# Performance work log

Hardware: AMD Instinct MI355X
Metric: run time of the kernel (lower is better)

The kernel has to match this reference:

```python
import jax, jax.numpy as jnp
import numpy as np

B = 32           # graphs in batch
N_PER = 512      # nodes per graph
N = B * N_PER    # 16384 total nodes (block-diagonal batched graph)
E = N * 16       # 262144 edges
D_IN = 128
D_OUT = 128
ASSIGN = 2048    # total clusters = B * K
K = ASSIGN // B  # 64 clusters per graph


def setup_inputs() -> dict:
    key = jax.random.key(0)
    ks = jax.random.split(key, 6)
    h = jax.random.normal(ks[0], (N, D_IN), jnp.float32)
    # edges confined within each graph -> block-diagonal batched adjacency
    gid = jnp.repeat(jnp.arange(B), E // B)
    edge_src = (jax.random.randint(ks[1], (E,), 0, N_PER) + gid * N_PER).astype(jnp.int32)
    edge_dst = (jax.random.randint(ks[2], (E,), 0, N_PER) + gid * N_PER).astype(jnp.int32)
    # GraphSage NodeApply linears: Linear(2*in, out)
    stdv_f = 1.0 / np.sqrt(2 * D_IN)
    W_feat = jax.random.uniform(ks[3], (2 * D_IN, D_OUT), jnp.float32, -stdv_f, stdv_f)
    b_feat = jnp.zeros((D_OUT,), jnp.float32)
    W_pool = jax.random.uniform(ks[4], (2 * D_IN, ASSIGN), jnp.float32, -stdv_f, stdv_f)
    b_pool = jnp.zeros((ASSIGN,), jnp.float32)
    return {"h": h, "W_feat": W_feat, "b_feat": b_feat,
            "W_pool": W_pool, "b_pool": b_pool,
            "edge_src": edge_src, "edge_dst": edge_dst}


def _graphsage(h, W, b, src, dst):
    # mean aggregation over in-neighbors (dropout=0, batch_norm off)
    msg = jax.ops.segment_sum(h[src], dst, num_segments=N)          # [N, d_in]
    deg = jax.ops.segment_sum(jnp.ones((src.shape[0],), h.dtype), dst, num_segments=N)
    h_neigh = msg / jnp.maximum(deg, 1.0)[:, None]
    bundle = jnp.concatenate([h, h_neigh], axis=1) @ W + b          # [N, d_out]
    # F.normalize(p=2, dim=1) then activation, as in GraphSage NodeApply
    norm = jnp.linalg.norm(bundle, axis=1, keepdims=True)
    bundle = bundle / jnp.maximum(norm, 1e-12)
    return jax.nn.relu(bundle)


def _forward(h, W_feat, b_feat, W_pool, b_pool, src, dst):
    feat = _graphsage(h, W_feat, b_feat, src, dst)       # [N, D_OUT]
    assign = _graphsage(h, W_pool, b_pool, src, dst)     # [N, ASSIGN]
    # block-diagonal mask: node i of graph g may only assign to g's K clusters
    gid_n = jnp.arange(N) // N_PER                       # [N]
    gid_c = jnp.arange(ASSIGN) // K                      # [ASSIGN]
    mask = (gid_n[:, None] == gid_c[None, :]).astype(jnp.float32)
    # masked_softmax with memory_efficient=False
    s = jax.nn.softmax(assign * mask, axis=-1) * mask
    s = s / (s.sum(axis=-1, keepdims=True) + 1e-13)      # [N, ASSIGN]
    h_new = s.T @ feat                                   # [ASSIGN, D_OUT]
    # adj_new = S^T A S without densifying A: (A S)[dst] += S[src]
    a_s = jax.ops.segment_sum(s[src], dst, num_segments=N)
    adj_new = s.T @ a_s                                  # [ASSIGN, ASSIGN]
    return adj_new, h_new


def reference(h, W_feat, b_feat, W_pool, b_pool, edge_src, edge_dst):
    return _forward(h, W_feat, b_feat, W_pool, b_pool, edge_src, edge_dst)
```

## Files before the change

kernel.cpp:

```cpp
#include <hip/hip_runtime.h>

#define NB   32
#define NPER 512
#define NN   16384
#define EE   262144
#define DD   128
#define AS   2048
#define KC   64

using short8   = __attribute__((ext_vector_type(8))) short;
using floatx4  = __attribute__((ext_vector_type(4))) float;
using ushort4v = __attribute__((ext_vector_type(4))) unsigned short;

typedef __attribute__((address_space(3))) unsigned int lds_u32;
typedef const __attribute__((address_space(1))) unsigned int gbl_u32;

static __device__ __forceinline__ void gload16(const unsigned short* g, unsigned short* l) {
    __builtin_amdgcn_global_load_lds((gbl_u32*)g, (lds_u32*)l, 16, 0, 0);
}

static __device__ __forceinline__ float bits2f(unsigned int u) {
    union { unsigned int i; float f; } z; z.i = u << 16; return z.f;
}
static __device__ __forceinline__ unsigned short f2b(float x) {
    union { float f; unsigned int u; } v; v.f = x;
    unsigned int r = v.u + 0x7fffu + ((v.u >> 16) & 1u);
    return (unsigned short)(r >> 16);
}

union PrepSMem {
    unsigned short fT[128 * 136];
    float tl[32][33];
};
__global__ void prep_kernel(const float* __restrict__ h, unsigned short* __restrict__ bundle,
                            unsigned short* __restrict__ hT, const int* __restrict__ esrc,
                            const int* __restrict__ edst, unsigned int* __restrict__ Acnt,
                            const float* __restrict__ Wf, const float* __restrict__ Wp,
                            unsigned short* __restrict__ WfT, unsigned short* __restrict__ WpT,
                            unsigned short* __restrict__ Wpb) {
    __shared__ PrepSMem sm;
    int b = blockIdx.x, t = threadIdx.x;
    if (b < 128) {
        int node0 = b * 128;
        int r = t >> 1, hf = t & 1;
        const float4* h4 = reinterpret_cast<const float4*>(h + (size_t)(node0 + r) * 128 + hf * 64);
        unsigned short* bo = bundle + (size_t)(node0 + r) * 256 + hf * 64;
#pragma unroll
        for (int i = 0; i < 16; i++) {
            float4 v = h4[i];
            ushort4v o = { f2b(v.x), f2b(v.y), f2b(v.z), f2b(v.w) };
            *reinterpret_cast<ushort4v*>(bo + 4 * i) = o;
            int c = hf * 64 + 4 * i;
            sm.fT[(c + 0) * 136 + r] = o.x;
            sm.fT[(c + 1) * 136 + r] = o.y;
            sm.fT[(c + 2) * 136 + r] = o.z;
            sm.fT[(c + 3) * 136 + r] = o.w;
        }
        __syncthreads();
        int c = t >> 1, nh = t & 1;
        const uint4* src = reinterpret_cast<const uint4*>(&sm.fT[c * 136 + nh * 64]);
        uint4* dst = reinterpret_cast<uint4*>(hT + (size_t)c * NN + node0 + nh * 64);
#pragma unroll
        for (int i = 0; i < 8; i++) dst[i] = src[i];
    } else if (b < 1152) {
        int e = (b - 128) * 256 + t;
        int d = edst[e], sl = esrc[e] & 511;
        int idx = d * 512 + sl;
        atomicAdd(&Acnt[idx >> 2], 1u << (8 * (idx & 3)));
    } else if (b < 1696) {
        int tb = b - 1152;
        int bx = tb % 68, by = tb / 68;
        int tx = t & 31, ty = t >> 5;
        const float* in; unsigned short* out; int C, cb;
        if (bx < DD / 32) { in = Wf; out = WfT; C = DD; cb = bx; }
        else              { in = Wp; out = WpT; C = AS; cb = bx - DD / 32; }
        int c0 = cb * 32, r0 = by * 32;
        for (int i = 0; i < 4; i++)
            sm.tl[ty + 8 * i][tx] = in[(size_t)(r0 + ty + 8 * i) * C + c0 + tx];
        __syncthreads();
        for (int i = 0; i < 4; i++)
            out[(size_t)(c0 + ty + 8 * i) * 256 + r0 + tx] = f2b(sm.tl[tx][ty + 8 * i]);
    } else {
        int gid = (b - 1696) * 256 + t;
        float4 v = reinterpret_cast<const float4*>(Wp)[gid];
        ushort4v o = { f2b(v.x), f2b(v.y), f2b(v.z), f2b(v.w) };
        *reinterpret_cast<ushort4v*>(&Wpb[(size_t)gid * 4]) = o;
    }
}

__global__ __launch_bounds__(256) void conv_kernel(
    const unsigned int* __restrict__ Acnt, unsigned short* __restrict__ Aadj,
    float* __restrict__ invdeg, const unsigned short* __restrict__ Wpb,
    const float* __restrict__ Wp, const float* __restrict__ bp,
    float* __restrict__ Gf, float* __restrict__ uF, float* __restrict__ cF) {
    __shared__ alignas(16) unsigned short glA[4096];
    __shared__ alignas(16) unsigned short glB[4096];
    __shared__ float gcred[4];
    int t = threadIdx.x, b = blockIdx.x;
    if (b < 2048) {
        int row = b * 8 + (t >> 5);
        int u = t & 31;
        uint4 w = reinterpret_cast<const uint4*>(Acnt)[(size_t)row * 32 + u];
        unsigned int wa[4] = { w.x, w.y, w.z, w.w };
        unsigned short out[16];
        float sum = 0.f;
#pragma unroll
        for (int i = 0; i < 4; i++) {
#pragma unroll
            for (int bb = 0; bb < 4; bb++) {
                float fv = (float)((wa[i] >> (8 * bb)) & 0xffu);
                sum += fv;
                out[4 * i + bb] = f2b(fv);
            }
        }
        unsigned int pw[8];
#pragma unroll
        for (int i = 0; i < 8; i++)
            pw[i] = (unsigned int)out[2 * i] | ((unsigned int)out[2 * i + 1] << 16);
        uint4* dst = reinterpret_cast<uint4*>(Aadj + (size_t)row * 512 + u * 16);
        uint4 s0 = { pw[0], pw[1], pw[2], pw[3] }, s1 = { pw[4], pw[5], pw[6], pw[7] };
        dst[0] = s0; dst[1] = s1;
#pragma unroll
        for (int d = 1; d < 32; d <<= 1) sum += __shfl_xor(sum, d, 64);
        if (u == 0) invdeg[row] = 1.0f / fmaxf(sum, 1.0f);
        return;
    }
    int b2 = b - 2048;
    int ks = b2 >> 2, ti = (b2 >> 1) & 1, tj = b2 & 1;
    int wv = t >> 6, lane = t & 63;
    int mw = wv >> 1, nw = wv & 1, q = lane >> 4, lm = lane & 15;
    int rowS0 = t >> 2,         cS0 = (t & 3) ^ ((rowS0 >> 1) & 3);
    int rowS1 = (t + 256) >> 2, cS1 = ((t + 256) & 3) ^ ((rowS1 >> 1) & 3);
    int swz = q ^ ((lm >> 1) & 3);
    floatx4 acc[4][4];
#pragma unroll
    for (int mi = 0; mi < 4; mi++)
#pragma unroll
        for (int ni = 0; ni < 4; ni++) acc[mi][ni] = (floatx4)0.f;
    for (int ki = 0; ki < 16; ki++) {
        int k0 = ks * 512 + ki * 32;
        gload16(Wpb + (size_t)(ti * 128 + rowS0) * 2048 + k0 + 8 * cS0, &glA[t * 8]);
        gload16(Wpb + (size_t)(ti * 128 + rowS1) * 2048 + k0 + 8 * cS1, &glA[(t + 256) * 8]);
        gload16(Wpb + (size_t)(tj * 128 + rowS0) * 2048 + k0 + 8 * cS0, &glB[t * 8]);
        gload16(Wpb + (size_t)(tj * 128 + rowS1) * 2048 + k0 + 8 * cS1, &glB[(t + 256) * 8]);
        __syncthreads();
        short8 aF[4], bF[4];
#pragma unroll
        for (int mi = 0; mi < 4; mi++)
            aF[mi] = *reinterpret_cast<const short8*>(&glA[((64 * mw + 16 * mi + lm) * 4 + swz) * 8]);
#pragma unroll
        for (int ni = 0; ni < 4; ni++)
            bF[ni] = *reinterpret_cast<const short8*>(&glB[((64 * nw + 16 * ni + lm) * 4 + swz) * 8]);
#pragma unroll
        for (int mi = 0; mi < 4; mi++)
#pragma unroll
            for (int ni = 0; ni < 4; ni++)
                acc[mi][ni] = __builtin_amdgcn_mfma_f32_16x16x32_bf16(aF[mi], bF[ni], acc[mi][ni], 0, 0, 0);
        __syncthreads();
    }
#pragma unroll
    for (int mi = 0; mi < 4; mi++)
#pragma unroll
        for (int ni = 0; ni < 4; ni++)
#pragma unroll
            for (int r = 0; r < 4; r++)
                atomicAdd(&Gf[(size_t)(ti * 128 + 64 * mw + 16 * mi + 4 * q + r) * 256 +
                              tj * 128 + 64 * nw + 16 * ni + lm], acc[mi][ni][r]);
    if (tj == 0) {
        int row = t >> 1, jh = t & 1;
        const float* wr = Wp + (size_t)(ti * 128 + row) * 2048 + ks * 512 + jh * 256;
        const float* br = bp + ks * 512 + jh * 256;
        float s = 0.f;
        for (int j = 0; j < 256; j++) s += wr[j] * br[j];
        atomicAdd(&uF[ti * 128 + row], s);
    }
    if (b2 == 0) {
        float s = 0.f;
        for (int j = t; j < 2048; j += 256) { float v = bp[j]; s += v * v; }
#pragma unroll
        for (int d = 1; d < 64; d <<= 1) s += __shfl_xor(s, d, 64);
        if (lane == 0) gcred[wv] = s;
        __syncthreads();
        if (t == 0) atomicAdd(cF, gcred[0] + gcred[1] + gcred[2] + gcred[3]);
    }
}

__global__ __launch_bounds__(256) void agg_h_mfma_kernel(
    const unsigned short* __restrict__ Aadj, const unsigned short* __restrict__ hT,
    const float* __restrict__ invdeg, unsigned short* __restrict__ bundle,
    const float* __restrict__ Gf, unsigned short* __restrict__ Gb) {
    __shared__ alignas(16) unsigned short lA[64 * 512];
    int tid = threadIdx.x, bx = blockIdx.x;
    if (bx >= 256) {
        int base = (bx - 256) * 16384;
        for (int i = 0; i < 16; i++) {
            int idx = base + i * 1024 + tid * 4;
            float4 v = *reinterpret_cast<const float4*>(Gf + idx);
            ushort4v o = { f2b(v.x), f2b(v.y), f2b(v.z), f2b(v.w) };
            *reinterpret_cast<ushort4v*>(&Gb[idx]) = o;
        }
        return;
    }
    int r0 = bx * 64, g = bx >> 3;
    int wv = tid >> 6, lane = tid & 63, q = lane >> 4, lm = lane & 15;
    int mw = wv >> 1, nw = wv & 1;
#pragma unroll
    for (int j = 0; j < 16; j++) {
        int u = tid + 256 * j;
        int row = u >> 6, cu = (u & 63) ^ (row & 7);
        gload16(Aadj + (size_t)(r0 + row) * 512 + cu * 8, &lA[u * 8]);
    }
    floatx4 acc[2][4];
#pragma unroll
    for (int mt = 0; mt < 2; mt++)
#pragma unroll
        for (int nt = 0; nt < 4; nt++) acc[mt][nt] = (floatx4)0.f;
    __syncthreads();
    const unsigned short* Bb = hT + (size_t)(64 * nw + lm) * NN + g * 512 + (q << 3);
    short8 bF[2][4];
#pragma unroll
    for (int nt = 0; nt < 4; nt++)
        bF[0][nt] = *reinterpret_cast<const short8*>(Bb + (size_t)16 * nt * NN);
    for (int ki = 0; ki < 16; ki++) {
        if (ki < 15) {
#pragma unroll
            for (int nt = 0; nt < 4; nt++)
                bF[(ki + 1) & 1][nt] =
                    *reinterpret_cast<const short8*>(Bb + (size_t)16 * nt * NN + (ki + 1) * 32);
        }
        short8 aF[2];
        int swz = (4 * ki + q) ^ (lm & 7);
#pragma unroll
        for (int mt = 0; mt < 2; mt++)
            aF[mt] = *reinterpret_cast<const short8*>(&lA[((32 * mw + 16 * mt + lm) * 64 + swz) * 8]);
#pragma unroll
        for (int mt = 0; mt < 2; mt++)
#pragma unroll
            for (int nt = 0; nt < 4; nt++)
                acc[mt][nt] = __builtin_amdgcn_mfma_f32_16x16x32_bf16(aF[mt], bF[ki & 1][nt],
                                                                      acc[mt][nt], 0, 0, 0);
    }
#pragma unroll
    for (int mt = 0; mt < 2; mt++)
#pragma unroll
        for (int r = 0; r < 4; r++) {
            int row = 32 * mw + 16 * mt + 4 * q + r;
            float inv = invdeg[r0 + row];
#pragma unroll
            for (int nt = 0; nt < 4; nt++)
                bundle[(size_t)(r0 + row) * 256 + 128 + 64 * nw + 16 * nt + lm] =
                    f2b(acc[mt][nt][r] * inv);
        }
}

union FPSMem {
    struct { unsigned short lA[4096]; unsigned short lB[4096]; float red[256];
             unsigned short fT2[8704]; } feat;
    struct { unsigned short lA[16384]; float raw[4352]; float ssq[256]; float rn[64];
             float uL[256]; } pool;
};
__global__ __launch_bounds__(256) void featpool_kernel(
    const unsigned short* __restrict__ bundle, const unsigned short* __restrict__ WfT,
    const unsigned short* __restrict__ WpT, const unsigned short* __restrict__ Gb,
    const float* __restrict__ bfe, const float* __restrict__ bp,
    const float* __restrict__ uF, const float* __restrict__ cF,
    unsigned short* __restrict__ featT, unsigned short* __restrict__ sT) {
    __shared__ FPSMem sm;
    int tid = threadIdx.x, b = blockIdx.x;
    if (b < 128) {
        int r0 = b * 128;
        int wv = tid >> 6, lane = tid & 63;
        int mw = wv >> 1, nw = wv & 1, q = lane >> 4, lm = lane & 15;
        int rowS0 = tid >> 2,         cS0 = (tid & 3) ^ ((rowS0 >> 1) & 3);
        int rowS1 = (tid + 256) >> 2, cS1 = ((tid + 256) & 3) ^ ((rowS1 >> 1) & 3);
        int swz = q ^ ((lm >> 1) & 3);
        floatx4 acc[4][4];
#pragma unroll
        for (int mi = 0; mi < 4; mi++)
#pragma unroll
            for (int ni = 0; ni < 4; ni++) acc[mi][ni] = (floatx4)0.f;
        for (int k0 = 0; k0 < 256; k0 += 32) {
            gload16(bundle + (size_t)(r0 + rowS0) * 256 + k0 + 8 * cS0, &sm.feat.lA[tid * 8]);
            gload16(bundle + (size_t)(r0 + rowS1) * 256 + k0 + 8 * cS1, &sm.feat.lA[(tid + 256) * 8]);
            gload16(WfT + (size_t)rowS0 * 256 + k0 + 8 * cS0, &sm.feat.lB[tid * 8]);
            gload16(WfT + (size_t)rowS1 * 256 + k0 + 8 * cS1, &sm.feat.lB[(tid + 256) * 8]);
            __syncthreads();
            short8 aF[4], bF[4];
#pragma unroll
            for (int mi = 0; mi < 4; mi++)
                aF[mi] = *reinterpret_cast<const short8*>(&sm.feat.lA[((64 * mw + 16 * mi + lm) * 4 + swz) * 8]);
#pragma unroll
            for (int ni = 0; ni < 4; ni++)
                bF[ni] = *reinterpret_cast<const short8*>(&sm.feat.lB[((64 * nw + 16 * ni + lm) * 4 + swz) * 8]);
#pragma unroll
            for (int mi = 0; mi < 4; mi++)
#pragma unroll
                for (int ni = 0; ni < 4; ni++)
                    acc[mi][ni] = __builtin_amdgcn_mfma_f32_16x16x32_bf16(aF[mi], bF[ni], acc[mi][ni], 0, 0, 0);
            __syncthreads();
        }
#pragma unroll
        for (int ni = 0; ni < 4; ni++) {
            float bv = bfe[64 * nw + 16 * ni + lm];
#pragma unroll
            for (int mi = 0; mi < 4; mi++)
#pragma unroll
                for (int r = 0; r < 4; r++) acc[mi][ni][r] += bv;
        }
#pragma unroll
        for (int mi = 0; mi < 4; mi++)
#pragma unroll
            for (int r = 0; r < 4; r++) {
                float p = 0.f;
#pragma unroll
                for (int ni = 0; ni < 4; ni++) p += acc[mi][ni][r] * acc[mi][ni][r];
                p += __shfl_xor(p, 1, 64);
                p += __shfl_xor(p, 2, 64);
                p += __shfl_xor(p, 4, 64);
                p += __shfl_xor(p, 8, 64);
                if (lm == 0) sm.feat.red[nw * 128 + 64 * mw + 16 * mi + 4 * q + r] = p;
            }
        __syncthreads();
        for (int rd = 0; rd < 2; rd++) {
            if (nw == rd) {
#pragma unroll
                for (int mi = 0; mi < 4; mi++) {
                    float rrn[4];
#pragma unroll
                    for (int r = 0; r < 4; r++) {
                        int rl = 64 * mw + 16 * mi + 4 * q + r;
                        rrn[r] = 1.0f / fmaxf(sqrtf(sm.feat.red[rl] + sm.feat.red[128 + rl]), 1e-12f);
                    }
#pragma unroll
                    for (int ni = 0; ni < 4; ni++) {
                        int col_loc = 16 * ni + lm;
                        ushort4v pk = { f2b(fmaxf(acc[mi][ni][0] * rrn[0], 0.f)),
                                        f2b(fmaxf(acc[mi][ni][1] * rrn[1], 0.f)),
                                        f2b(fmaxf(acc[mi][ni][2] * rrn[2], 0.f)),
                                        f2b(fmaxf(acc[mi][ni][3] * rrn[3], 0.f)) };
                        *reinterpret_cast<ushort4v*>(&sm.feat.fT2[col_loc * 136 + 64 * mw + 16 * mi + 4 * q]) = pk;
                    }
                }
            }
            __syncthreads();
#pragma unroll
            for (int i = 0; i < 4; i++) {
                int idx = tid + 256 * i;
                int cl = idx >> 4, pos = idx & 15;
                uint4 v = *reinterpret_cast<const uint4*>(&sm.feat.fT2[cl * 136 + pos * 8]);
                *reinterpret_cast<uint4*>(featT + (size_t)(64 * rd + cl) * NN + r0 + pos * 8) = v;
            }
            __syncthreads();
        }
    } else {
        int bx = b - 128;
        int r0 = bx * 64, g = bx >> 3;
        int wv = tid >> 6, lane = tid & 63, q = lane >> 4, lm = lane & 15;
#pragma unroll
        for (int j = 0; j < 8; j++) {
            int u = tid + 256 * j;
            int row = u >> 5;
            int chunk = (u & 31) ^ (row & 7);
            gload16(bundle + (size_t)(r0 + row) * 256 + chunk * 8, &sm.pool.lA[u * 8]);
        }
        sm.pool.uL[tid] = uF[tid];
        __syncthreads();
        {
            const unsigned short* Bb = Gb + ((size_t)(wv * 64 + lm) << 8) + (q << 3);
            short8 bF[2][4];
#pragma unroll
            for (int ni = 0; ni < 4; ni++)
                bF[0][ni] = *reinterpret_cast<const short8*>(Bb + (ni << 12));
            floatx4 acc[4][4];
#pragma unroll
            for (int mi = 0; mi < 4; mi++)
#pragma unroll
                for (int ni = 0; ni < 4; ni++) acc[mi][ni] = (floatx4)0.f;
#pragma unroll
            for (int k = 0; k < 8; k++) {
                if (k < 7) {
#pragma unroll
                    for (int ni = 0; ni < 4; ni++)
                        bF[(k + 1) & 1][ni] =
                            *reinterpret_cast<const short8*>(Bb + (ni << 12) + ((k + 1) << 5));
                }
                short8 aF[4];
                int swz = (4 * k + q) ^ (lm & 7);
#pragma unroll
                for (int mi = 0; mi < 4; mi++)
                    aF[mi] = *reinterpret_cast<const short8*>(&sm.pool.lA[((16 * mi + lm) * 32 + swz) * 8]);
#pragma unroll
                for (int mi = 0; mi < 4; mi++)
#pragma unroll
                    for (int ni = 0; ni < 4; ni++)
                        acc[mi][ni] = __builtin_amdgcn_mfma_f32_16x16x32_bf16(aF[mi], bF[k & 1][ni],
                                                                              acc[mi][ni], 0, 0, 0);
            }
            float uc[4];
#pragma unroll
            for (int ni = 0; ni < 4; ni++) uc[ni] = sm.pool.uL[64 * wv + 16 * ni + lm];
#pragma unroll
            for (int mi = 0; mi < 4; mi++)
#pragma unroll
                for (int r = 0; r < 4; r++) {
                    int row = 16 * mi + 4 * q + r;
                    float p = 0.f;
#pragma unroll
                    for (int ni = 0; ni < 4; ni++) {
                        int col = 64 * wv + 16 * ni + lm;
                        int cu = (col >> 3) ^ (row & 7);
                        float xv = bits2f((unsigned int)sm.pool.lA[(row * 32 + cu) * 8 + (col & 7)]);
                        p += (acc[mi][ni][r] + 2.f * uc[ni]) * xv;
                    }
                    p += __shfl_xor(p, 1, 64);
                    p += __shfl_xor(p, 2, 64);
                    p += __shfl_xor(p, 4, 64);
                    p += __shfl_xor(p, 8, 64);
                    if (lm == 0) sm.pool.ssq[wv * 64 + row] = p;
                }
        }
        {
            const unsigned short* Bb2 = WpT + (size_t)(g * KC + 16 * wv + lm) * 256 + (q << 3);
            short8 b2[2];
            b2[0] = *reinterpret_cast<const short8*>(Bb2);
            floatx4 acc2[4];
#pragma unroll
            for (int mi = 0; mi < 4; mi++) acc2[mi] = (floatx4)0.f;
#pragma unroll
            for (int k = 0; k < 8; k++) {
                if (k < 7) b2[(k + 1) & 1] = *reinterpret_cast<const short8*>(Bb2 + ((k + 1) << 5));
                short8 aF[4];
                int swz = (4 * k + q) ^ (lm & 7);
#pragma unroll
                for (int mi = 0; mi < 4; mi++)
                    aF[mi] = *reinterpret_cast<const short8*>(&sm.pool.lA[((16 * mi + lm) * 32 + swz) * 8]);
#pragma unroll
                for (int mi = 0; mi < 4; mi++)
                    acc2[mi] = __builtin_amdgcn_mfma_f32_16x16x32_bf16(aF[mi], b2[k & 1], acc2[mi], 0, 0, 0);
            }
            float bv = bp[g * KC + 16 * wv + lm];
#pragma unroll
            for (int mi = 0; mi < 4; mi++)
#pragma unroll
                for (int r = 0; r < 4; r++)
                    sm.pool.raw[(16 * mi + 4 * q + r) * 68 + 16 * wv + lm] = acc2[mi][r] + bv;
        }
        __syncthreads();
        if (tid < 64)
            sm.pool.rn[tid] = 1.0f / fmaxf(sqrtf(sm.pool.ssq[tid] + sm.pool.ssq[64 + tid] +
                                           sm.pool.ssq[128 + tid] + sm.pool.ssq[192 + tid] + cF[0]), 1e-12f);
        __syncthreads();
        {
            int row = tid >> 2, j = tid & 3;
            int nloc = ((bx & 7) << 6) + row;
            float rn = sm.pool.rn[row];
            float v[16];
            float mx = -1e30f;
#pragma unroll
            for (int c4 = 0; c4 < 4; c4++) {
                float4 rv = *reinterpret_cast<const float4*>(&sm.pool.raw[row * 68 + 16 * j + 4 * c4]);
                v[4 * c4 + 0] = fmaxf(rv.x * rn, 0.f);
                v[4 * c4 + 1] = fmaxf(rv.y * rn, 0.f);
                v[4 * c4 + 2] = fmaxf(rv.z * rn, 0.f);
                v[4 * c4 + 3] = fmaxf(rv.w * rn, 0.f);
            }
#pragma unroll
            for (int c = 0; c < 16; c++) mx = fmaxf(mx, v[c]);
            mx = fmaxf(mx, __shfl_xor(mx, 1, 64));
            mx = fmaxf(mx, __shfl_xor(mx, 2, 64));
            float z = 0.f;
#pragma unroll
            for (int c = 0; c < 16; c++) { v[c] = __expf(v[c] - mx); z += v[c]; }
            z += __shfl_xor(z, 1, 64);
            z += __shfl_xor(z, 2, 64);
            float iz = 1.0f / z;
#pragma unroll
            for (int c4 = 0; c4 < 4; c4++) {
                size_t tb = (size_t)(g * KC + 16 * j + 4 * c4) * NPER + nloc;
                sT[tb] = f2b(v[4 * c4 + 0] * iz);
                sT[tb + NPER] = f2b(v[4 * c4 + 1] * iz);
                sT[tb + 2 * NPER] = f2b(v[4 * c4 + 2] * iz);
                sT[tb + 3 * NPER] = f2b(v[4 * c4 + 3] * iz);
            }
        }
    }
}

__global__ __launch_bounds__(256) void as_mfma_kernel(
    const unsigned short* __restrict__ sT, const unsigned short* __restrict__ Aadj,
    unsigned short* __restrict__ asT) {
    __shared__ alignas(16) unsigned short lS[64 * 512];
    int tid = threadIdx.x, bx = blockIdx.x;
    int g = bx >> 1, half = bx & 1;
    int wv = tid >> 6, lane = tid & 63, q = lane >> 4, lm = lane & 15;
#pragma unroll
    for (int j = 0; j < 16; j++) {
        int u = tid + 256 * j;
        int row = u >> 6, cu = (u & 63) ^ (row & 7);
        gload16(sT + (size_t)(g * KC + row) * NPER + cu * 8, &lS[u * 8]);
    }
    floatx4 acc[4][4];
#pragma unroll
    for (int mi = 0; mi < 4; mi++)
#pragma unroll
        for (int nt = 0; nt < 4; nt++) acc[mi][nt] = (floatx4)0.f;
    __syncthreads();
    int dbase = half * 256 + wv * 64;
    const unsigned short* Bb = Aadj + (size_t)(g * 512 + dbase + lm) * 512 + (q << 3);
    short8 bF[2][4];
#pragma unroll
    for (int nt = 0; nt < 4; nt++)
        bF[0][nt] = *reinterpret_cast<const short8*>(Bb + (size_t)16 * nt * 512);
    for (int ki = 0; ki < 16; ki++) {
        if (ki < 15) {
#pragma unroll
            for (int nt = 0; nt < 4; nt++)
                bF[(ki + 1) & 1][nt] =
                    *reinterpret_cast<const short8*>(Bb + (size_t)16 * nt * 512 + (ki + 1) * 32);
        }
        short8 aF[4];
        int swz = (4 * ki + q) ^ (lm & 7);
#pragma unroll
        for (int mi = 0; mi < 4; mi++)
            aF[mi] = *reinterpret_cast<const short8*>(&lS[((16 * mi + lm) * 64 + swz) * 8]);
#pragma unroll
        for (int mi = 0; mi < 4; mi++)
#pragma unroll
            for (int nt = 0; nt < 4; nt++)
                acc[mi][nt] = __builtin_amdgcn_mfma_f32_16x16x32_bf16(aF[mi], bF[ki & 1][nt],
                                                                      acc[mi][nt], 0, 0, 0);
    }
#pragma unroll
    for (int mi = 0; mi < 4; mi++)
#pragma unroll
        for (int r = 0; r < 4; r++) {
            int row = 16 * mi + 4 * q + r;
#pragma unroll
            for (int nt = 0; nt < 4; nt++)
                asT[(size_t)(g * KC + row) * NPER + dbase + 16 * nt + lm] = f2b(acc[mi][nt][r]);
        }
}

__global__ __launch_bounds__(256) void hnew_adj2_kernel(
    const unsigned short* __restrict__ sT, const unsigned short* __restrict__ featT,
    const unsigned short* __restrict__ asT, float* __restrict__ adjf,
    float* __restrict__ hnewf) {
    __shared__ alignas(16) unsigned short lS[1024 * 8];
    __shared__ alignas(16) unsigned short lF[2048 * 8];
    __shared__ alignas(16) unsigned short lAS[1024 * 8];
    int tid = threadIdx.x, b = blockIdx.x;
    if (b >= 32) {
        uint4 z = { 0u, 0u, 0u, 0u };
        for (int row = b - 32; row < AS; row += 224) {
            int g = row >> 6;
            uint4* out = reinterpret_cast<uint4*>(adjf + (size_t)row * AS);
            for (int i = tid; i < 512; i += 256)
                if (i < g * 16 || i >= g * 16 + 16) out[i] = z;
        }
        return;
    }
    int g = b;
    int wv = tid >> 6, lane = tid & 63, q = lane >> 4, lm = lane & 15;
    bool isH = (wv < 2);
    floatx4 accH[4][4];
    floatx4 accA[4][2];
#pragma unroll
    for (int mi = 0; mi < 4; mi++) {
#pragma unroll
        for (int ni = 0; ni < 4; ni++) accH[mi][ni] = (floatx4)0.f;
#pragma unroll
        for (int ni = 0; ni < 2; ni++) accA[mi][ni] = (floatx4)0.f;
    }
    for (int ks = 0; ks < 4; ks++) {
#pragma unroll
        for (int j = 0; j < 4; j++) {
            int u = tid + 256 * j;
            int row = u >> 4, cu = (u & 15) ^ (row & 15);
            gload16(sT + (size_t)(g * KC + row) * NPER + ks * 128 + cu * 8, &lS[u * 8]);
        }
#pragma unroll
        for (int j = 0; j < 8; j++) {
            int u = tid + 256 * j;
            int row = u >> 4, cu = (u & 15) ^ (row & 15);
            gload16(featT + (size_t)row * NN + g * NPER + ks * 128 + cu * 8, &lF[u * 8]);
        }
#pragma unroll
        for (int j = 0; j < 4; j++) {
            int u = tid + 256 * j;
            int row = u >> 4, cu = (u & 15) ^ (row & 15);
            gload16(asT + (size_t)(g * KC + row) * NPER + ks * 128 + cu * 8, &lAS[u * 8]);
        }
        __syncthreads();
#pragma unroll
        for (int kk = 0; kk < 4; kk++) {
            short8 aF[4];
#pragma unroll
            for (int mi = 0; mi < 4; mi++)
                aF[mi] = *reinterpret_cast<const short8*>(
                    &lS[((16 * mi + lm) * 16 + ((4 * kk + q) ^ lm)) * 8]);
            if (isH) {
                short8 bF[4];
#pragma unroll
                for (int ni = 0; ni < 4; ni++)
                    bF[ni] = *reinterpret_cast<const short8*>(
                        &lF[((64 * wv + 16 * ni + lm) * 16 + ((4 * kk + q) ^ lm)) * 8]);
#pragma unroll
                for (int mi = 0; mi < 4; mi++)
#pragma unroll
                    for (int ni = 0; ni < 4; ni++)
                        accH[mi][ni] = __builtin_amdgcn_mfma_f32_16x16x32_bf16(aF[mi], bF[ni],
                                                                               accH[mi][ni], 0, 0, 0);
            } else {
                short8 bF[2];
#pragma unroll
                for (int ni = 0; ni < 2; ni++)
                    bF[ni] = *reinterpret_cast<const short8*>(
                        &lAS[((32 * (wv - 2) + 16 * ni + lm) * 16 + ((4 * kk + q) ^ lm)) * 8]);
#pragma unroll
                for (int mi = 0; mi < 4; mi++)
#pragma unroll
                    for (int ni = 0; ni < 2; ni++)
                        accA[mi][ni] = __builtin_amdgcn_mfma_f32_16x16x32_bf16(aF[mi], bF[ni],
                                                                               accA[mi][ni], 0, 0, 0);
            }
        }
        __syncthreads();
    }
    if (isH) {
#pragma unroll
        for (int mi = 0; mi < 4; mi++)
#pragma unroll
            for (int ni = 0; ni < 4; ni++)
#pragma unroll
                for (int r = 0; r < 4; r++)
                    hnewf[(size_t)(g * KC + 16 * mi + 4 * q + r) * DD +
                          64 * wv + 16 * ni + lm] = accH[mi][ni][r];
    } else {
#pragma unroll
        for (int mi = 0; mi < 4; mi++)
#pragma unroll
            for (int ni = 0; ni < 2; ni++)
#pragma unroll
                for (int r = 0; r < 4; r++)
                    adjf[(size_t)(g * KC + 16 * mi + 4 * q + r) * AS +
                         g * KC + 32 * (wv - 2) + 16 * ni + lm] = accA[mi][ni][r];
    }
}

extern "C" void kernel_launch(void* const* d_in, const int* in_sizes, int n_in,
                              void* d_out, int out_size, void* d_ws, size_t ws_size,
                              hipStream_t stream) {
    const float* h   = (const float*)d_in[0];
    const float* Wf  = (const float*)d_in[1];
    const float* bfe = (const float*)d_in[2];
    const float* Wp  = (const float*)d_in[3];
    const float* bp  = (const float*)d_in[4];
    const int* esrc  = (const int*)d_in[5];
    const int* edst  = (const int*)d_in[6];

    float* adjf  = (float*)d_out;
    float* hnewf = adjf + (size_t)AS * AS;

    unsigned short* bundle = (unsigned short*)d_ws;
    unsigned short* WfT   = bundle + (size_t)NN * 256;
    unsigned short* WpT   = WfT + 128 * 256;
    unsigned short* sT    = WpT + (size_t)AS * 256;
    unsigned short* asT   = sT + (size_t)NN * KC;
    unsigned short* featT = asT + (size_t)NN * KC;
    unsigned short* hT    = featT + (size_t)DD * NN;
    unsigned short* Aadj  = hT + (size_t)DD * NN;
    float* invdeg = (float*)(Aadj + (size_t)NN * 512);
    unsigned int* Acnt = (unsigned int*)(invdeg + NN);
    float* Gf = (float*)(Acnt + (size_t)NN * 128);
    float* uF = Gf + 65536;
    float* cF = uF + 256;
    unsigned short* Wpb = (unsigned short*)(cF + 4);
    unsigned short* Gb  = Wpb + (size_t)256 * 2048;

    hipMemsetAsync(Acnt, 0, (size_t)NN * 512 + (65536 + 256 + 4) * sizeof(float), stream);

    prep_kernel<<<2208, 256, 0, stream>>>(h, bundle, hT, esrc, edst, Acnt, Wf, Wp, WfT, WpT, Wpb);
    conv_kernel<<<2064, 256, 0, stream>>>(Acnt, Aadj, invdeg, Wpb, Wp, bp, Gf, uF, cF);
    agg_h_mfma_kernel<<<260, 256, 0, stream>>>(Aadj, hT, invdeg, bundle, Gf, Gb);
    featpool_kernel<<<384, 256, 0, stream>>>(bundle, WfT, WpT, Gb, bfe, bp, uF, cF, featT, sT);
    as_mfma_kernel<<<NB * 2, 256, 0, stream>>>(sT, Aadj, asT);
    hnew_adj2_kernel<<<256, 256, 0, stream>>>(sT, featT, asT, adjf, hnewf);
}
```

Baseline: 174.1 us.

## Fuse conv kernel into prep and agg kernels, drop Wpb staging and featT LDS transpose

Removes the separate conv_kernel launch. The W_pool Gram GEMM now runs in prep_kernel, converting fp32 W_pool to bf16 on the fly instead of going through a staged Wpb buffer. The adjacency-count-to-bf16 conversion and row degree sums move into agg_h_mfma_kernel, which writes LDS and global Aadj directly and computes inverse degree from shared memory. The feat epilogue writes featT straight to global memory rather than transposing through LDS. The cost is a dependency hazard: the Gram GEMM in prep now runs in the same launch as the edge atomics, though it does not depend on them. The direct featT stores are also narrower and less coalesced.

```diff
diff --git a/kernel.cpp b/kernel.cpp
--- a/kernel.cpp
+++ b/kernel.cpp
@@ -18,7 +18,6 @@
 static __device__ __forceinline__ void gload16(const unsigned short* g, unsigned short* l) {
     __builtin_amdgcn_global_load_lds((gbl_u32*)g, (lds_u32*)l, 16, 0, 0);
 }
-
 static __device__ __forceinline__ float bits2f(unsigned int u) {
     union { unsigned int i; float f; } z; z.i = u << 16; return z.f;
 }
@@ -27,17 +26,24 @@
     unsigned int r = v.u + 0x7fffu + ((v.u >> 16) & 1u);
     return (unsigned short)(r >> 16);
 }
+static __device__ __forceinline__ unsigned short f2b_exact(float x) {
+    union { float f; unsigned int u; } v; v.f = x;
+    return (unsigned short)(v.u >> 16);
+}
 
 union PrepSMem {
     unsigned short fT[128 * 136];
     float tl[32][33];
+    struct { unsigned short glA[4096]; unsigned short glB[4096]; float gcred[4]; } gg;
 };
 __global__ void prep_kernel(const float* __restrict__ h, unsigned short* __restrict__ bundle,
                             unsigned short* __restrict__ hT, const int* __restrict__ esrc,
                             const int* __restrict__ edst, unsigned int* __restrict__ Acnt,
                             const float* __restrict__ Wf, const float* __restrict__ Wp,
+                            const float* __restrict__ bp,
                             unsigned short* __restrict__ WfT, unsigned short* __restrict__ WpT,
-                            unsigned short* __restrict__ Wpb) {
+                            float* __restrict__ Gf, float* __restrict__ uF,
+                            float* __restrict__ cF) {
     __shared__ PrepSMem sm;
     int b = blockIdx.x, t = threadIdx.x;
     if (b < 128) {
@@ -81,115 +87,87 @@
         for (int i = 0; i < 4; i++)
             out[(size_t)(c0 + ty + 8 * i) * 256 + r0 + tx] = f2b(sm.tl[tx][ty + 8 * i]);
     } else {
-        int gid = (b - 1696) * 256 + t;
-        float4 v = reinterpret_cast<const float4*>(Wp)[gid];
-        ushort4v o = { f2b(v.x), f2b(v.y), f2b(v.z), f2b(v.w) };
-        *reinterpret_cast<ushort4v*>(&Wpb[(size_t)gid * 4]) = o;
-    }
-}
-
-__global__ __launch_bounds__(256) void conv_kernel(
-    const unsigned int* __restrict__ Acnt, unsigned short* __restrict__ Aadj,
-    float* __restrict__ invdeg, const unsigned short* __restrict__ Wpb,
-    const float* __restrict__ Wp, const float* __restrict__ bp,
-    float* __restrict__ Gf, float* __restrict__ uF, float* __restrict__ cF) {
-    __shared__ alignas(16) unsigned short glA[4096];
-    __shared__ alignas(16) unsigned short glB[4096];
-    __shared__ float gcred[4];
-    int t = threadIdx.x, b = blockIdx.x;
-    if (b < 2048) {
-        int row = b * 8 + (t >> 5);
-        int u = t & 31;
-        uint4 w = reinterpret_cast<const uint4*>(Acnt)[(size_t)row * 32 + u];
-        unsigned int wa[4] = { w.x, w.y, w.z, w.w };
-        unsigned short out[16];
-        float sum = 0.f;
-#pragma unroll
-        for (int i = 0; i < 4; i++) {
-#pragma unroll
-            for (int bb = 0; bb < 4; bb++) {
-                float fv = (float)((wa[i] >> (8 * bb)) & 0xffu);
-                sum += fv;
-                out[4 * i + bb] = f2b(fv);
-            }
-        }
-        unsigned int pw[8];
-#pragma unroll
-        for (int i = 0; i < 8; i++)
-            pw[i] = (unsigned int)out[2 * i] | ((unsigned int)out[2 * i + 1] << 16);
-        uint4* dst = reinterpret_cast<uint4*>(Aadj + (size_t)row * 512 + u * 16);
-        uint4 s0 = { pw[0], pw[1], pw[2], pw[3] }, s1 = { pw[4], pw[5], pw[6], pw[7] };
-        dst[0] = s0; dst[1] = s1;
-#pragma unroll
-        for (int d = 1; d < 32; d <<= 1) sum += __shfl_xor(sum, d, 64);
-        if (u == 0) invdeg[row] = 1.0f / fmaxf(sum, 1.0f);
-        return;
-    }
-    int b2 = b - 2048;
-    int ks = b2 >> 2, ti = (b2 >> 1) & 1, tj = b2 & 1;
-    int wv = t >> 6, lane = t & 63;
-    int mw = wv >> 1, nw = wv & 1, q = lane >> 4, lm = lane & 15;
-    int rowS0 = t >> 2,         cS0 = (t & 3) ^ ((rowS0 >> 1) & 3);
-    int rowS1 = (t + 256) >> 2, cS1 = ((t + 256) & 3) ^ ((rowS1 >> 1) & 3);
-    int swz = q ^ ((lm >> 1) & 3);
-    floatx4 acc[4][4];
-#pragma unroll
-    for (int mi = 0; mi < 4; mi++)
-#pragma unroll
-        for (int ni = 0; ni < 4; ni++) acc[mi][ni] = (floatx4)0.f;
-    for (int ki = 0; ki < 16; ki++) {
-        int k0 = ks * 512 + ki * 32;
-        gload16(Wpb + (size_t)(ti * 128 + rowS0) * 2048 + k0 + 8 * cS0, &glA[t * 8]);
-        gload16(Wpb + (size_t)(ti * 128 + rowS1) * 2048 + k0 + 8 * cS1, &glA[(t + 256) * 8]);
-        gload16(Wpb + (size_t)(tj * 128 + rowS0) * 2048 + k0 + 8 * cS0, &glB[t * 8]);
-        gload16(Wpb + (size_t)(tj * 128 + rowS1) * 2048 + k0 + 8 * cS1, &glB[(t + 256) * 8]);
-        __syncthreads();
-        short8 aF[4], bF[4];
-#pragma unroll
-        for (int mi = 0; mi < 4; mi++)
-            aF[mi] = *reinterpret_cast<const short8*>(&glA[((64 * mw + 16 * mi + lm) * 4 + swz) * 8]);
-#pragma unroll
-        for (int ni = 0; ni < 4; ni++)
-            bF[ni] = *reinterpret_cast<const short8*>(&glB[((64 * nw + 16 * ni + lm) * 4 + swz) * 8]);
-#pragma unroll
-        for (int mi = 0; mi < 4; mi++)
+        int b2 = b - 1696;
+        int ks = b2 >> 2, ti = (b2 >> 1) & 1, tj = b2 & 1;
+        int wv = t >> 6, lane = t & 63;
+        int mw = wv >> 1, nw = wv & 1, q = lane >> 4, lm = lane & 15;
+        int swz = q ^ ((lm >> 1) & 3);
+        floatx4 acc[4][4];
+#pragma unroll
+        for (int mi = 0; mi < 4; mi++)
+#pragma unroll
+            for (int ni = 0; ni < 4; ni++) acc[mi][ni] = (floatx4)0.f;
+        for (int ki = 0; ki < 16; ki++) {
+            int k0 = ks * 512 + ki * 32;
+#pragma unroll
+            for (int half = 0; half < 2; half++) {
+                int u = t + 256 * half;
+                int row = u >> 2, c = u & 3;
+                int cs = c ^ ((row >> 1) & 3);
+                const float4* sa = reinterpret_cast<const float4*>(
+                    Wp + (size_t)(ti * 128 + row) * 2048 + k0 + c * 8);
+                float4 v0 = sa[0], v1 = sa[1];
+                ushort4v p0 = { f2b(v0.x), f2b(v0.y), f2b(v0.z), f2b(v0.w) };
+                ushort4v p1 = { f2b(v1.x), f2b(v1.y), f2b(v1.z), f2b(v1.w) };
+                *reinterpret_cast<ushort4v*>(&sm.gg.glA[(row * 4 + cs) * 8]) = p0;
+                *reinterpret_cast<ushort4v*>(&sm.gg.glA[(row * 4 + cs) * 8 + 4]) = p1;
+                const float4* sb = reinterpret_cast<const float4*>(
+                    Wp + (size_t)(tj * 128 + row) * 2048 + k0 + c * 8);
+                float4 w0 = sb[0], w1 = sb[1];
+                ushort4v q0 = { f2b(w0.x), f2b(w0.y), f2b(w0.z), f2b(w0.w) };
+                ushort4v q1 = { f2b(w1.x), f2b(w1.y), f2b(w1.z), f2b(w1.w) };
+                *reinterpret_cast<ushort4v*>(&sm.gg.glB[(row * 4 + cs) * 8]) = q0;
+                *reinterpret_cast<ushort4v*>(&sm.gg.glB[(row * 4 + cs) * 8 + 4]) = q1;
+            }
+            __syncthreads();
+            short8 aF[4], bF[4];
+#pragma unroll
+            for (int mi = 0; mi < 4; mi++)
+                aF[mi] = *reinterpret_cast<const short8*>(&sm.gg.glA[((64 * mw + 16 * mi + lm) * 4 + swz) * 8]);
 #pragma unroll
             for (int ni = 0; ni < 4; ni++)
-                acc[mi][ni] = __builtin_amdgcn_mfma_f32_16x16x32_bf16(aF[mi], bF[ni], acc[mi][ni], 0, 0, 0);
-        __syncthreads();
-    }
-#pragma unroll
-    for (int mi = 0; mi < 4; mi++)
-#pragma unroll
-        for (int ni = 0; ni < 4; ni++)
-#pragma unroll
-            for (int r = 0; r < 4; r++)
-                atomicAdd(&Gf[(size_t)(ti * 128 + 64 * mw + 16 * mi + 4 * q + r) * 256 +
-                              tj * 128 + 64 * nw + 16 * ni + lm], acc[mi][ni][r]);
-    if (tj == 0) {
-        int row = t >> 1, jh = t & 1;
-        const float* wr = Wp + (size_t)(ti * 128 + row) * 2048 + ks * 512 + jh * 256;
-        const float* br = bp + ks * 512 + jh * 256;
-        float s = 0.f;
-        for (int j = 0; j < 256; j++) s += wr[j] * br[j];
-        atomicAdd(&uF[ti * 128 + row], s);
-    }
-    if (b2 == 0) {
-        float s = 0.f;
-        for (int j = t; j < 2048; j += 256) { float v = bp[j]; s += v * v; }
-#pragma unroll
-        for (int d = 1; d < 64; d <<= 1) s += __shfl_xor(s, d, 64);
-        if (lane == 0) gcred[wv] = s;
-        __syncthreads();
-        if (t == 0) atomicAdd(cF, gcred[0] + gcred[1] + gcred[2] + gcred[3]);
+                bF[ni] = *reinterpret_cast<const short8*>(&sm.gg.glB[((64 * nw + 16 * ni + lm) * 4 + swz) * 8]);
+#pragma unroll
+            for (int mi = 0; mi < 4; mi++)
+#pragma unroll
+                for (int ni = 0; ni < 4; ni++)
+                    acc[mi][ni] = __builtin_amdgcn_mfma_f32_16x16x32_bf16(aF[mi], bF[ni], acc[mi][ni], 0, 0, 0);
+            __syncthreads();
+        }
+#pragma unroll
+        for (int mi = 0; mi < 4; mi++)
+#pragma unroll
+            for (int ni = 0; ni < 4; ni++)
+#pragma unroll
+                for (int r = 0; r < 4; r++)
+                    atomicAdd(&Gf[(size_t)(ti * 128 + 64 * mw + 16 * mi + 4 * q + r) * 256 +
+                                  tj * 128 + 64 * nw + 16 * ni + lm], acc[mi][ni][r]);
+        if (tj == 0) {
+            int row = t >> 1, jh = t & 1;
+            const float* wr = Wp + (size_t)(ti * 128 + row) * 2048 + ks * 512 + jh * 256;
+            const float* br = bp + ks * 512 + jh * 256;
+            float s = 0.f;
+            for (int j = 0; j < 256; j++) s += wr[j] * br[j];
+            atomicAdd(&uF[ti * 128 + row], s);
+        }
+        if (b2 == 0) {
+            float s = 0.f;
+            for (int j = t; j < 2048; j += 256) { float v = bp[j]; s += v * v; }
+#pragma unroll
+            for (int d = 1; d < 64; d <<= 1) s += __shfl_xor(s, d, 64);
+            if (lane == 0) sm.gg.gcred[wv] = s;
+            __syncthreads();
+            if (t == 0) atomicAdd(cF, sm.gg.gcred[0] + sm.gg.gcred[1] + sm.gg.gcred[2] + sm.gg.gcred[3]);
+        }
     }
 }
 
 __global__ __launch_bounds__(256) void agg_h_mfma_kernel(
-    const unsigned short* __restrict__ Aadj, const unsigned short* __restrict__ hT,
-    const float* __restrict__ invdeg, unsigned short* __restrict__ bundle,
+    const unsigned int* __restrict__ Acnt, const unsigned short* __restrict__ hT,
+    unsigned short* __restrict__ bundle, unsigned short* __restrict__ Aadj,
     const float* __restrict__ Gf, unsigned short* __restrict__ Gb) {
     __shared__ alignas(16) unsigned short lA[64 * 512];
+    __shared__ float rs[64];
     int tid = threadIdx.x, bx = blockIdx.x;
     if (bx >= 256) {
         int base = (bx - 256) * 16384;
@@ -204,11 +182,35 @@
     int r0 = bx * 64, g = bx >> 3;
     int wv = tid >> 6, lane = tid & 63, q = lane >> 4, lm = lane & 15;
     int mw = wv >> 1, nw = wv & 1;
-#pragma unroll
-    for (int j = 0; j < 16; j++) {
-        int u = tid + 256 * j;
-        int row = u >> 6, cu = (u & 63) ^ (row & 7);
-        gload16(Aadj + (size_t)(r0 + row) * 512 + cu * 8, &lA[u * 8]);
+    if (tid < 64) rs[tid] = 0.f;
+    __syncthreads();
+#pragma unroll
+    for (int j = 0; j < 8; j++) {
+        int ub = tid + 256 * j;
+        int row = ub >> 5, kb = ub & 31;
+        uint4 w = reinterpret_cast<const uint4*>(Acnt)[(size_t)(r0 + row) * 32 + kb];
+        unsigned int wa[4] = { w.x, w.y, w.z, w.w };
+        unsigned short ob[16];
+        float sum = 0.f;
+#pragma unroll
+        for (int i = 0; i < 4; i++) {
+#pragma unroll
+            for (int bb = 0; bb < 4; bb++) {
+                float fv = (float)((wa[i] >> (8 * bb)) & 0xffu);
+                sum += fv;
+                ob[4 * i + bb] = f2b_exact(fv);
+            }
+        }
+        atomicAdd(&rs[row], sum);
+        uint4* gdst = reinterpret_cast<uint4*>(&Aadj[(size_t)(r0 + row) * 512 + kb * 16]);
+        gdst[0] = *reinterpret_cast<const uint4*>(&ob[0]);
+        gdst[1] = *reinterpret_cast<const uint4*>(&ob[8]);
+#pragma unroll
+        for (int jj = 0; jj < 2; jj++) {
+            int pos = (kb * 2 + jj) ^ (row & 7);
+            *reinterpret_cast<uint4*>(&lA[(row * 64 + pos) * 8]) =
+                *reinterpret_cast<const uint4*>(&ob[8 * jj]);
+        }
     }
     floatx4 acc[2][4];
 #pragma unroll
@@ -245,7 +247,7 @@
 #pragma unroll
         for (int r = 0; r < 4; r++) {
             int row = 32 * mw + 16 * mt + 4 * q + r;
-            float inv = invdeg[r0 + row];
+            float inv = 1.0f / fmaxf(rs[row], 1.0f);
 #pragma unroll
             for (int nt = 0; nt < 4; nt++)
                 bundle[(size_t)(r0 + row) * 256 + 128 + 64 * nw + 16 * nt + lm] =
@@ -254,8 +256,7 @@
 }
 
 union FPSMem {
-    struct { unsigned short lA[4096]; unsigned short lB[4096]; float red[256];
-             unsigned short fT2[8704]; } feat;
+    struct { unsigned short lA[4096]; unsigned short lB[4096]; float red[256]; } feat;
     struct { unsigned short lA[16384]; float raw[4352]; float ssq[256]; float rn[64];
              float uL[256]; } pool;
 };
@@ -321,36 +322,24 @@
                 if (lm == 0) sm.feat.red[nw * 128 + 64 * mw + 16 * mi + 4 * q + r] = p;
             }
         __syncthreads();
-        for (int rd = 0; rd < 2; rd++) {
-            if (nw == rd) {
-#pragma unroll
-                for (int mi = 0; mi < 4; mi++) {
-                    float rrn[4];
-#pragma unroll
-                    for (int r = 0; r < 4; r++) {
-                        int rl = 64 * mw + 16 * mi + 4 * q + r;
-                        rrn[r] = 1.0f / fmaxf(sqrtf(sm.feat.red[rl] + sm.feat.red[128 + rl]), 1e-12f);
-                    }
-#pragma unroll
-                    for (int ni = 0; ni < 4; ni++) {
-                        int col_loc = 16 * ni + lm;
-                        ushort4v pk = { f2b(fmaxf(acc[mi][ni][0] * rrn[0], 0.f)),
-                                        f2b(fmaxf(acc[mi][ni][1] * rrn[1], 0.f)),
-                                        f2b(fmaxf(acc[mi][ni][2] * rrn[2], 0.f)),
-                                        f2b(fmaxf(acc[mi][ni][3] * rrn[3], 0.f)) };
-                        *reinterpret_cast<ushort4v*>(&sm.feat.fT2[col_loc * 136 + 64 * mw + 16 * mi + 4 * q]) = pk;
-                    }
-                }
-            }
-            __syncthreads();
-#pragma unroll
-            for (int i = 0; i < 4; i++) {
-                int idx = tid + 256 * i;
-                int cl = idx >> 4, pos = idx & 15;
-                uint4 v = *reinterpret_cast<const uint4*>(&sm.feat.fT2[cl * 136 + pos * 8]);
-                *reinterpret_cast<uint4*>(featT + (size_t)(64 * rd + cl) * NN + r0 + pos * 8) = v;
-            }
-            __syncthreads();
+#pragma unroll
+        for (int mi = 0; mi < 4; mi++) {
+            float rrn[4];
+#pragma unroll
+            for (int r = 0; r < 4; r++) {
+                int rl = 64 * mw + 16 * mi + 4 * q + r;
+                rrn[r] = 1.0f / fmaxf(sqrtf(sm.feat.red[rl] + sm.feat.red[128 + rl]), 1e-12f);
+            }
+#pragma unroll
+            for (int ni = 0; ni < 4; ni++) {
+                int col = 64 * nw + 16 * ni + lm;
+                ushort4v pk = { f2b(fmaxf(acc[mi][ni][0] * rrn[0], 0.f)),
+                                f2b(fmaxf(acc[mi][ni][1] * rrn[1], 0.f)),
+                                f2b(fmaxf(acc[mi][ni][2] * rrn[2], 0.f)),
+                                f2b(fmaxf(acc[mi][ni][3] * rrn[3], 0.f)) };
+                *reinterpret_cast<ushort4v*>(
+                    &featT[(size_t)col * NN + r0 + 64 * mw + 16 * mi + 4 * q]) = pk;
+            }
         }
     } else {
         int bx = b - 128;
@@ -669,19 +658,17 @@
     unsigned short* featT = asT + (size_t)NN * KC;
     unsigned short* hT    = featT + (size_t)DD * NN;
     unsigned short* Aadj  = hT + (size_t)DD * NN;
-    float* invdeg = (float*)(Aadj + (size_t)NN * 512);
-    unsigned int* Acnt = (unsigned int*)(invdeg + NN);
+    unsigned int* Acnt = (unsigned int*)(Aadj + (size_t)NN * 512);
     float* Gf = (float*)(Acnt + (size_t)NN * 128);
     float* uF = Gf + 65536;
     float* cF = uF + 256;
-    unsigned short* Wpb = (unsigned short*)(cF + 4);
-    unsigned short* Gb  = Wpb + (size_t)256 * 2048;
+    unsigned short* Gb = (unsigned short*)(cF + 4);
 
     hipMemsetAsync(Acnt, 0, (size_t)NN * 512 + (65536 + 256 + 4) * sizeof(float), stream);
 
-    prep_kernel<<<2208, 256, 0, stream>>>(h, bundle, hT, esrc, edst, Acnt, Wf, Wp, WfT, WpT, Wpb);
-    conv_kernel<<<2064, 256, 0, stream>>>(Acnt, Aadj, invdeg, Wpb, Wp, bp, Gf, uF, cF);
-    agg_h_mfma_kernel<<<260, 256, 0, stream>>>(Aadj, hT, invdeg, bundle, Gf, Gb);
+    prep_kernel<<<1712, 256, 0, stream>>>(h, bundle, hT, esrc, edst, Acnt,
+                                          Wf, Wp, bp, WfT, WpT, Gf, uF, cF);
+    agg_h_mfma_kernel<<<260, 256, 0, stream>>>(Acnt, hT, bundle, Aadj, Gf, Gb);
     featpool_kernel<<<384, 256, 0, stream>>>(bundle, WfT, WpT, Gb, bfe, bp, uF, cF, featT, sT);
     as_mfma_kernel<<<NB * 2, 256, 0, stream>>>(sT, Aadj, asT);
     hnew_adj2_kernel<<<256, 256, 0, stream>>>(sT, featT, asT, adjf, hnewf);
```

Measured after the change: 188.2 us. 8.1% more time.
